# Performance work log

Hardware: AMD Instinct MI355X
Metric: run time of the kernel (lower is better)

Reference implementation:

```python
import jax, jax.numpy as jnp
import numpy as np
import math

N, E, H, NB, NL, NG, NELEM = 50000, 800000, 64, 8, 2, 64, 100
CUTOFF = 5.0


def _lin(k, fin, fout):
    kw, kb = jax.random.split(k)
    bound = 1.0 / math.sqrt(fin)
    w = jax.random.uniform(kw, (fin, fout), jnp.float32, -bound, bound)
    b = jax.random.uniform(kb, (fout,), jnp.float32, -bound, bound)
    return w, b


def setup_inputs() -> dict:
    key = jax.random.key(0)
    ks = jax.random.split(key, 12)
    z = jax.random.randint(ks[0], (N,), 0, NELEM)
    pos = jax.random.normal(ks[1], (N, 3), jnp.float32)
    edge_index = jax.random.randint(ks[2], (2, E), 0, N)
    batch = jnp.sort(jax.random.randint(ks[3], (N,), 0, NG))
    embed = jax.random.normal(ks[4], (NELEM, H), jnp.float32)
    # stacked per-interaction MLP params, leading dim = NL
    msg_w1, msg_b1, msg_w2, msg_b2 = [], [], [], []
    upd_w1, upd_b1, upd_w2, upd_b2 = [], [], [], []
    for l in range(NL):
        kl = jax.random.fold_in(ks[5], l)
        k1, k2, k3, k4 = jax.random.split(kl, 4)
        w, b = _lin(k1, 2 * H + NB, H); msg_w1.append(w); msg_b1.append(b)
        w, b = _lin(k2, H, H); msg_w2.append(w); msg_b2.append(b)
        w, b = _lin(k3, 2 * H, H); upd_w1.append(w); upd_b1.append(b)
        w, b = _lin(k4, H, H); upd_w2.append(w); upd_b2.append(b)
    eh_w1, eh_b1 = _lin(ks[6], H, H)
    eh_w2, eh_b2 = _lin(ks[7], H, 1)
    return {
        "z": z, "pos": pos, "edge_index": edge_index, "batch": batch,
        "embed": embed,
        "msg_w1": jnp.stack(msg_w1), "msg_b1": jnp.stack(msg_b1),
        "msg_w2": jnp.stack(msg_w2), "msg_b2": jnp.stack(msg_b2),
        "upd_w1": jnp.stack(upd_w1), "upd_b1": jnp.stack(upd_b1),
        "upd_w2": jnp.stack(upd_w2), "upd_b2": jnp.stack(upd_b2),
        "eh_w1": eh_w1, "eh_b1": eh_b1, "eh_w2": eh_w2, "eh_b2": eh_b2,
    }


def _mace_energy(pos, embed, msg_w1, msg_b1, msg_w2, msg_b2,
                 upd_w1, upd_b1, upd_w2, upd_b2,
                 eh_w1, eh_b1, eh_w2, eh_b2,
                 z, edge_index, batch):
    row, col = edge_index[0], edge_index[1]
    edge_vec = pos[row] - pos[col]                      # (E,3)
    d = jnp.linalg.norm(edge_vec, axis=-1)              # (E,)
    env = jnp.where(d < CUTOFF,
                    jnp.cos(d * (math.pi / (2 * CUTOFF))) ** 2,
                    0.0)
    freqs = jnp.arange(1, NB + 1, dtype=pos.dtype) * (math.pi / CUTOFF)
    d_safe = jnp.where(d > 0, d, 1.0)[:, None]
    edge_attr = jnp.sin(freqs * d[:, None]) / d_safe * env[:, None]  # (E,NB)

    x = embed[z]                                        # (N,H)
    for l in range(NL):
        # PyG source_to_target: x_j = x[row], x_i = x[col], aggregate at col
        msg_in = jnp.concatenate([x[col], x[row], edge_attr], axis=-1)  # (E,2H+NB)
        m = jax.nn.silu(msg_in @ msg_w1[l] + msg_b1[l]) @ msg_w2[l] + msg_b2[l]
        agg = jax.ops.segment_sum(m, col, num_segments=N)               # (N,H)
        u_in = jnp.concatenate([x, agg], axis=-1)
        upd = jax.nn.silu(u_in @ upd_w1[l] + upd_b1[l]) @ upd_w2[l] + upd_b2[l]
        x = x + upd

    atomic_e = jax.nn.silu(x @ eh_w1 + eh_b1) @ eh_w2 + eh_b2           # (N,1)
    energy = jax.ops.segment_sum(atomic_e, batch, num_segments=NG)      # (NG,1)
    return energy.squeeze(-1)


def reference(z, pos, edge_index, batch, embed,
              msg_w1, msg_b1, msg_w2, msg_b2,
              upd_w1, upd_b1, upd_w2, upd_b2,
              eh_w1, eh_b1, eh_w2, eh_b2):
    return _mace_energy(pos, embed, msg_w1, msg_b1, msg_w2, msg_b2,
                        upd_w1, upd_b1, upd_w2, upd_b2,
                        eh_w1, eh_b1, eh_w2, eh_b2,
                        z, edge_index, batch)
```

## Files before the change

kernel.cpp:

```cpp
#include <hip/hip_runtime.h>
#include <math.h>

#define NN 50000
#define EE 800000
#define HH 64
#define NBASIS 8
#define NLAYER 2
#define NGRAPH 64
#define NBLK1 49

using half2_t = decltype(__builtin_amdgcn_cvt_pkrtz(0.0f, 0.0f));
typedef _Float16 f16x8 __attribute__((ext_vector_type(8)));
typedef float f32x4 __attribute__((ext_vector_type(4)));

union U4H8 { uint4 u; f16x8 h; };

__device__ __forceinline__ float silu_f(float v) {
    return v * (1.0f / (1.0f + __expf(-v)));
}

__device__ __forceinline__ unsigned pk2(float a, float b) {
    union { half2_t h; unsigned u; } x;
    x.h = __builtin_amdgcn_cvt_pkrtz(a, b);
    return x.u;
}

__device__ __forceinline__ half2_t u2h(unsigned u) {
    union { unsigned u; half2_t h; } x; x.u = u; return x.h;
}

__global__ __launch_bounds__(256) void prep_k(
    const int* __restrict__ z, const float* __restrict__ embed,
    unsigned* __restrict__ xh,
    const float* __restrict__ msg_w1, const float* __restrict__ msg_w2,
    const float* __restrict__ msg_b2,
    const float* __restrict__ upd_w1, const float* __restrict__ upd_w2,
    const float* __restrict__ eh_w1,
    unsigned* __restrict__ w1t, float* __restrict__ vbuf,
    unsigned* __restrict__ w1tu, unsigned* __restrict__ w2tu,
    unsigned* __restrict__ ehw1t,
    const int* __restrict__ ecol, int* __restrict__ deg,
    float4* __restrict__ agg4)
{
    int b = blockIdx.x;
    if (b < 6250) {
        int idx = b * 256 + threadIdx.x;
        int n = idx >> 5;
        int p = idx & 31;
        const float2* er = (const float2*)(embed + ((size_t)z[n] << 6));
        float2 v = er[p];
        xh[idx] = pk2(v.x, v.y);
    } else if (b < 6362) {
        int idx = (b - 6250) * 256 + threadIdx.x;
        if (idx < 10240) {
            int l = idx / 5120, rem = idx % 5120;
            int f = rem / 80, kp = rem % 80;
            const float* w = msg_w1 + (size_t)l * 136 * 64;
            unsigned v = 0;
            if (kp < 68) v = pk2(w[(2*kp)*64 + f], w[(2*kp+1)*64 + f]);
            w1t[idx] = v;
        } else if (idx < 14336) {
        } else if (idx < 22528) {
            int j = idx - 14336;
            int l = j / 4096, rem = j % 4096;
            int f = rem >> 6, kp = rem & 63;
            const float* w = upd_w1 + (size_t)l * 128 * 64;
            unsigned outv;
            if (kp < 32) {
                outv = pk2(w[(2*kp)*64 + f], w[(2*kp+1)*64 + f]);
            } else {
                const float* w2m = msg_w2 + (size_t)l * 64 * 64;
                int j0 = 2 * kp - 64;
                float v0 = 0.0f, v1 = 0.0f;
                for (int k = 0; k < 64; ++k) {
                    float wa = w[(64 + k) * 64 + f];
                    v0 += w2m[j0 * 64 + k]       * wa;
                    v1 += w2m[(j0 + 1) * 64 + k] * wa;
                }
                outv = pk2(v0, v1);
                if (kp == 63) {
                    const float* b2m = msg_b2 + (size_t)l * 64;
                    float s = 0.0f;
                    for (int k = 0; k < 64; ++k)
                        s += b2m[k] * w[(64 + k) * 64 + f];
                    vbuf[l * 64 + f] = s;
                }
            }
            w1tu[j] = outv;
        } else if (idx < 26624) {
            int j = idx - 22528;
            int l = j / 2048, rem = j % 2048;
            int n = rem / 32, kp = rem % 32;
            const float* w = upd_w2 + (size_t)l * 64 * 64;
            w2tu[j] = pk2(w[(2*kp)*64 + n], w[(2*kp+1)*64 + n]);
        } else if (idx < 28672) {
            int j = idx - 26624;
            int f = j / 32, kp = j % 32;
            ehw1t[j] = pk2(eh_w1[(2*kp)*64 + f], eh_w1[(2*kp+1)*64 + f]);
        }
    } else if (b < 9487) {
        int e = (b - 6362) * 256 + threadIdx.x;
        if (e < EE) atomicAdd(&deg[ecol[e]], 1);
    } else {
        int idx = (b - 9487) * 256 + threadIdx.x;
        if (idx < NN * 16) {
            float4 z4; z4.x = z4.y = z4.z = z4.w = 0.0f;
            agg4[idx] = z4;
        }
    }
}

__global__ __launch_bounds__(1024) void scan1_k(
    const int* __restrict__ deg, int* __restrict__ cursor,
    int* __restrict__ bsum)
{
    __shared__ int wsum[16];
    int t = threadIdx.x, lane = t & 63, wave = t >> 6;
    int i = blockIdx.x * 1024 + t;
    int v = (i < NN) ? deg[i] : 0;
    int s = v;
#pragma unroll
    for (int off = 1; off < 64; off <<= 1) {
        int tv = __shfl_up(s, off, 64);
        if (lane >= off) s += tv;
    }
    if (lane == 63) wsum[wave] = s;
    __syncthreads();
    if (wave == 0) {
        int ws = (lane < 16) ? wsum[lane] : 0;
        int ss = ws;
#pragma unroll
        for (int off = 1; off < 16; off <<= 1) {
            int tv = __shfl_up(ss, off, 64);
            if (lane >= off) ss += tv;
        }
        if (lane < 16) wsum[lane] = ss - ws;
    }
    __syncthreads();
    int excl = wsum[wave] + s - v;
    if (i < NN) cursor[i] = excl;
    if (t == 1023) bsum[blockIdx.x] = excl + v;
}

__global__ __launch_bounds__(64) void scan2_k(int* __restrict__ bsum)
{
    int lane = threadIdx.x;
    int v = (lane < NBLK1) ? bsum[lane] : 0;
    int s = v;
#pragma unroll
    for (int off = 1; off < 64; off <<= 1) {
        int tv = __shfl_up(s, off, 64);
        if (lane >= off) s += tv;
    }
    if (lane < NBLK1) bsum[lane] = s - v;
}

__global__ __launch_bounds__(256) void scatter_k(
    const int* __restrict__ erow, const int* __restrict__ ecol,
    const float* __restrict__ pos,
    int* __restrict__ cursor, const int* __restrict__ bsum,
    uint2* __restrict__ edgeS)
{
    int e = blockIdx.x * 256 + threadIdx.x;
    if (e >= EE) return;
    int c = ecol[e], r = erow[e];
    int slot = atomicAdd(&cursor[c], 1) + bsum[c >> 10];
    float dx = pos[3*r]   - pos[3*c];
    float dy = pos[3*r+1] - pos[3*c+1];
    float dz = pos[3*r+2] - pos[3*c+2];
    float d = sqrtf(dx*dx + dy*dy + dz*dz);
    uint2 v;
    v.x = ((unsigned)r << 16) | (unsigned)c;
    v.y = __float_as_uint(d);
    edgeS[slot] = v;
}

__global__ __launch_bounds__(256, 4) void msg_k(
    const uint2* __restrict__ edgeS,
    const unsigned* __restrict__ xh,
    const unsigned* __restrict__ w1t, const float* __restrict__ b1,
    float* __restrict__ agg)
{
    __shared__ unsigned earrT[4][4 * 64];
    __shared__ int ckey_s[4][64];
    __shared__ float Mbuf[4][64 * 34];

    const int wid  = threadIdx.x >> 6;
    const int lane = threadIdx.x & 63;
    const int q = lane >> 4, n15 = lane & 15;
    const size_t base = (size_t)blockIdx.x * 256 + wid * 64;

    uint2 ev = edgeS[base + lane];
    int myrow = (int)(ev.x >> 16);
    int mykey = (int)(ev.x & 0xffffu);
    ckey_s[wid][lane] = mykey;

    int cn[4], rn[4];
#pragma unroll
    for (int nt = 0; nt < 4; ++nt) {
        cn[nt] = __shfl(mykey, nt * 16 + n15, 64);
        rn[nt] = __shfl(myrow, nt * 16 + n15, 64);
    }

    U4H8 bfr[2][4];
#pragma unroll
    for (int nt = 0; nt < 4; ++nt) {
        const uint4* rp = (const uint4*)(xh + ((size_t)rn[nt] << 5));
        bfr[0][nt].u = rp[q];
        bfr[1][nt].u = rp[4 + q];
    }

    {
        float d = __uint_as_float(ev.y);
        float env = 0.0f;
        if (d < 5.0f) {
            float cv = __cosf(d * 0.31415926535897932f);
            env = cv * cv;
        }
        float scale = (d > 0.0f) ? (env / d) : env;
        float ea[NBASIS];
#pragma unroll
        for (int k = 0; k < NBASIS; ++k)
            ea[k] = __sinf((float)(k + 1) * 0.62831853071795865f * d) * scale;
#pragma unroll
        for (int p = 0; p < 4; ++p)
            earrT[wid][p * 64 + lane] = pk2(ea[2*p], ea[2*p+1]);
    }
    int pkk = __shfl_up(mykey, 1, 64);
    unsigned long long bmask = __ballot(lane > 0 && mykey != pkk);
    unsigned m32 = (unsigned)(bmask >> (lane & 32));
    __syncthreads();

    f32x4 acc1[4][4];
#pragma unroll
    for (int mt = 0; mt < 4; ++mt) {
        f32x4 binit = *(const f32x4*)(b1 + mt * 16 + q * 4);
#pragma unroll
        for (int nt = 0; nt < 4; ++nt) acc1[mt][nt] = binit;
    }
#pragma unroll
    for (int ks = 0; ks < 5; ++ks) {
        U4H8 bfk[4];
#pragma unroll
        for (int nt = 0; nt < 4; ++nt) {
            if (ks == 4) {
                int eB = nt * 16 + n15;
                unsigned e0 = earrT[wid][0 * 64 + eB];
                unsigned e1 = earrT[wid][1 * 64 + eB];
                unsigned e2 = earrT[wid][2 * 64 + eB];
                unsigned e3 = earrT[wid][3 * 64 + eB];
                bfk[nt].u.x = (q == 0) ? e0 : 0u;
                bfk[nt].u.y = (q == 0) ? e1 : 0u;
                bfk[nt].u.z = (q == 0) ? e2 : 0u;
                bfk[nt].u.w = (q == 0) ? e3 : 0u;
            } else if (ks < 2) {
                bfk[nt].u = ((const uint4*)(xh + ((size_t)cn[nt] << 5)))[ks * 4 + q];
            } else {
                bfk[nt] = bfr[ks - 2][nt];
            }
        }
#pragma unroll
        for (int mt = 0; mt < 4; ++mt) {
            U4H8 af;
            af.u = *(const uint4*)(w1t + (size_t)(mt * 16 + n15) * 80 + ks * 16 + q * 4);
#pragma unroll
            for (int nt = 0; nt < 4; ++nt)
                acc1[mt][nt] = __builtin_amdgcn_mfma_f32_16x16x32_f16(
                    af.h, bfk[nt].h, acc1[mt][nt], 0, 0, 0);
        }
    }

#pragma unroll
    for (int hf = 0; hf < 2; ++hf) {
#pragma unroll
        for (int mh = 0; mh < 2; ++mh) {
            int mt = 2 * hf + mh;
#pragma unroll
            for (int nt = 0; nt < 4; ++nt) {
                int eb = nt * 16 + n15;
#pragma unroll
                for (int r = 0; r < 4; ++r)
                    Mbuf[wid][eb * 34 + mh * 16 + q * 4 + r] =
                        silu_f(acc1[mt][nt][r]);
            }
        }
        __syncthreads();
        {
            int cl = lane & 31, st = lane >> 5;
            int ebase = 32 * st;
            float run = Mbuf[wid][ebase * 34 + cl];
            int runkey = ckey_s[wid][ebase];
            bool atstart = true;
#pragma unroll
            for (int i = 1; i < 32; ++i) {
                float v = Mbuf[wid][(ebase + i) * 34 + cl];
                if ((m32 >> i) & 1u) {
                    float* dst = agg + ((size_t)runkey << 6) + hf * 32 + cl;
                    if (atstart) atomicAdd(dst, run); else *dst = run;
                    runkey = ckey_s[wid][ebase + i]; atstart = false;
                    run = v;
                } else {
                    run += v;
                }
            }
            atomicAdd(agg + ((size_t)runkey << 6) + hf * 32 + cl, run);
        }
        __syncthreads();
    }
}

__global__ __launch_bounds__(256) void upd_k(
    unsigned* __restrict__ xh,
    float* __restrict__ agg,
    const unsigned* __restrict__ w1t, const float* __restrict__ b1,
    const float* __restrict__ vb, const int* __restrict__ deg,
    const unsigned* __restrict__ w2t, const float* __restrict__ b2,
    const unsigned* __restrict__ ehw1t, const float* __restrict__ ehb1,
    const float* __restrict__ ehw2, const float* __restrict__ ehb2,
    const int* __restrict__ batch, float* __restrict__ energy,
    int do_zero, int do_head)
{
    __shared__ unsigned MU[4][16 * 33];
    __shared__ float esum[NGRAPH];

    const int tid = threadIdx.x;
    const int wid = tid >> 6;
    const int lane = tid & 63;
    const int q = lane >> 4, n15 = lane & 15;
    const int base16 = blockIdx.x * 64 + wid * 16;

    if (do_head) {
        if (tid < NGRAPH) esum[tid] = 0.0f;
        __syncthreads();
    }

    int nodeB = base16 + n15;
    int ncB = (nodeB < NN) ? nodeB : (NN - 1);

    float degf = (float)deg[ncB];
    f32x4 acc1[4];
#pragma unroll
    for (int mt = 0; mt < 4; ++mt) {
        f32x4 bi = *(const f32x4*)(b1 + mt * 16 + q * 4);
        f32x4 vv = *(const f32x4*)(vb + mt * 16 + q * 4);
#pragma unroll
        for (int r = 0; r < 4; ++r) bi[r] = fmaf(degf, vv[r], bi[r]);
        acc1[mt] = bi;
    }
#pragma unroll
    for (int ks = 0; ks < 4; ++ks) {
        U4H8 bfk;
        if (ks < 2) {
            bfk.u = ((const uint4*)(xh + ((size_t)ncB << 5)))[ks * 4 + q];
        } else {
            const float4* ap = (const float4*)(agg + ((size_t)ncB << 6));
            int o = (ks - 2) * 8 + 2 * q;
            float4 a0 = ap[o], a1 = ap[o + 1];
            bfk.u.x = pk2(a0.x, a0.y); bfk.u.y = pk2(a0.z, a0.w);
            bfk.u.z = pk2(a1.x, a1.y); bfk.u.w = pk2(a1.z, a1.w);
        }
#pragma unroll
        for (int mt = 0; mt < 4; ++mt) {
            U4H8 af;
            af.u = *(const uint4*)(w1t + (size_t)(mt * 16 + n15) * 64 + ks * 16 + q * 4);
            acc1[mt] = __builtin_amdgcn_mfma_f32_16x16x32_f16(
                af.h, bfk.h, acc1[mt], 0, 0, 0);
        }
    }

    unsigned psrc[4][2];
#pragma unroll
    for (int mt = 0; mt < 4; ++mt) {
        psrc[mt][0] = pk2(silu_f(acc1[mt][0]), silu_f(acc1[mt][1]));
        psrc[mt][1] = pk2(silu_f(acc1[mt][2]), silu_f(acc1[mt][3]));
    }

    f32x4 acc2[4];
#pragma unroll
    for (int nt = 0; nt < 4; ++nt) {
        float b2v = b2[nt * 16 + n15];
        acc2[nt][0] = b2v; acc2[nt][1] = b2v; acc2[nt][2] = b2v; acc2[nt][3] = b2v;
    }
#pragma unroll
    for (int ks2 = 0; ks2 < 2; ++ks2) {
        unsigned tmp[4];
#pragma unroll
        for (int jr = 0; jr < 4; ++jr) {
            int srcl = (2 * (q & 1) + (jr >> 1)) * 16 + n15;
            unsigned v0 = (unsigned)__shfl((int)psrc[2 * ks2][jr & 1], srcl, 64);
            unsigned v1 = (unsigned)__shfl((int)psrc[2 * ks2 + 1][jr & 1], srcl, 64);
            tmp[jr] = (q >> 1) ? v1 : v0;
        }
        U4H8 pf;
        pf.u.x = tmp[0]; pf.u.y = tmp[1]; pf.u.z = tmp[2]; pf.u.w = tmp[3];
#pragma unroll
        for (int nt = 0; nt < 4; ++nt) {
            U4H8 wb;
            wb.u = *(const uint4*)(w2t + (size_t)(nt * 16 + n15) * 32 + ks2 * 16 + q * 4);
            acc2[nt] = __builtin_amdgcn_mfma_f32_16x16x32_f16(
                pf.h, wb.h, acc2[nt], 0, 0, 0);
        }
    }

#pragma unroll
    for (int nt = 0; nt < 4; ++nt) {
#pragma unroll
        for (int r = 0; r < 4; ++r) {
            int node = base16 + 4 * q + r;
            float vnew = 0.0f;
            if (node < NN) {
                unsigned pu = xh[((size_t)node << 5) + (unsigned)((nt * 16 + n15) >> 1)];
                half2_t hp = u2h(pu);
                float vold = (n15 & 1) ? (float)hp[1] : (float)hp[0];
                vnew = vold + acc2[nt][r];
            }
            float vpart = __shfl_xor(vnew, 1, 64);
            if ((n15 & 1) == 0) {
                unsigned pv = pk2(vnew, vpart);
                int pidx = nt * 8 + (n15 >> 1);
                MU[wid][(4 * q + r) * 33 + pidx] = pv;
                if (node < NN) xh[((size_t)node << 5) + pidx] = pv;
            }
        }
    }

    if (do_zero) {
        if (nodeB < NN) {
            float4 z4; z4.x = z4.y = z4.z = z4.w = 0.0f;
            float4* ap = (float4*)(agg + ((size_t)nodeB << 6));
            ap[2*q] = z4; ap[2*q + 1] = z4;
            ap[8 + 2*q] = z4; ap[8 + 2*q + 1] = z4;
        }
    }

    if (do_head) {
        __syncthreads();
        f32x4 acch[4];
#pragma unroll
        for (int mt = 0; mt < 4; ++mt)
            acch[mt] = *(const f32x4*)(ehb1 + mt * 16 + q * 4);
#pragma unroll
        for (int ks = 0; ks < 2; ++ks) {
            U4H8 bfk;
            bfk.u.x = MU[wid][n15 * 33 + ks * 16 + 4 * q + 0];
            bfk.u.y = MU[wid][n15 * 33 + ks * 16 + 4 * q + 1];
            bfk.u.z = MU[wid][n15 * 33 + ks * 16 + 4 * q + 2];
            bfk.u.w = MU[wid][n15 * 33 + ks * 16 + 4 * q + 3];
#pragma unroll
            for (int mt = 0; mt < 4; ++mt) {
                U4H8 af;
                af.u = *(const uint4*)(ehw1t + (size_t)(mt * 16 + n15) * 32 + ks * 16 + q * 4);
                acch[mt] = __builtin_amdgcn_mfma_f32_16x16x32_f16(
                    af.h, bfk.h, acch[mt], 0, 0, 0);
            }
        }
        f32x4 wv[4];
#pragma unroll
        for (int mt = 0; mt < 4; ++mt)
            wv[mt] = *(const f32x4*)(ehw2 + mt * 16 + q * 4);
        float e = 0.0f;
#pragma unroll
        for (int mt = 0; mt < 4; ++mt)
#pragma unroll
            for (int r = 0; r < 4; ++r)
                e = fmaf(silu_f(acch[mt][r]), wv[mt][r], e);
        e += __shfl_xor(e, 16, 64);
        e += __shfl_xor(e, 32, 64);
        if (q == 0) {
            int node = base16 + n15;
            if (node < NN) atomicAdd(&esum[batch[node]], e + ehb2[0]);
        }
        __syncthreads();
        if (tid < NGRAPH) {
            float v = esum[tid];
            if (v != 0.0f) atomicAdd(energy + tid, v);
        }
    }
}

extern "C" void kernel_launch(void* const* d_in, const int* in_sizes, int n_in,
                              void* d_out, int out_size, void* d_ws, size_t ws_size,
                              hipStream_t stream) {
    const int*   z       = (const int*)  d_in[0];
    const float* pos     = (const float*)d_in[1];
    const int*   eidx    = (const int*)  d_in[2];
    const int*   batch   = (const int*)  d_in[3];
    const float* embed   = (const float*)d_in[4];
    const float* msg_w1  = (const float*)d_in[5];
    const float* msg_b1  = (const float*)d_in[6];
    const float* msg_w2  = (const float*)d_in[7];
    const float* msg_b2  = (const float*)d_in[8];
    const float* upd_w1  = (const float*)d_in[9];
    const float* upd_b1  = (const float*)d_in[10];
    const float* upd_w2  = (const float*)d_in[11];
    const float* upd_b2  = (const float*)d_in[12];
    const float* eh_w1   = (const float*)d_in[13];
    const float* eh_b1   = (const float*)d_in[14];
    const float* eh_w2   = (const float*)d_in[15];
    const float* eh_b2   = (const float*)d_in[16];

    const int* erow = eidx;
    const int* ecol = eidx + EE;

    float*    agg    = (float*)d_ws;
    unsigned* xh     = (unsigned*)(agg + (size_t)NN * HH);
    int*      deg    = (int*)(xh + (size_t)NN * 32);
    int*      cursor = deg + NN;
    int*      bsum   = cursor + NN;
    uint2*    edgeS  = (uint2*)(bsum + 64);
    unsigned* w1t    = (unsigned*)(edgeS + EE);
    unsigned* w2t    = w1t + NLAYER * 64 * 80;
    unsigned* w1tu   = w2t + NLAYER * 64 * 32;
    unsigned* w2tu   = w1tu + NLAYER * 64 * 64;
    unsigned* ehw1t  = w2tu + NLAYER * 64 * 32;
    float*    vbuf   = (float*)w2t;
    float*    energy = (float*)d_out;

    (void)hipMemsetAsync(energy, 0, NGRAPH * sizeof(float), stream);
    (void)hipMemsetAsync(deg, 0, NN * sizeof(int), stream);

    prep_k<<<12612, 256, 0, stream>>>(
        z, embed, xh,
        msg_w1, msg_w2, msg_b2, upd_w1, upd_w2, eh_w1,
        w1t, vbuf, w1tu, w2tu, ehw1t,
        ecol, deg, (float4*)agg);

    scan1_k<<<NBLK1, 1024, 0, stream>>>(deg, cursor, bsum);
    scan2_k<<<1, 64, 0, stream>>>(bsum);
    scatter_k<<<(EE + 255) / 256, 256, 0, stream>>>(
        erow, ecol, pos, cursor, bsum, edgeS);

    for (int l = 0; l < NLAYER; ++l) {
        msg_k<<<EE / 256, 256, 0, stream>>>(
            edgeS, xh,
            w1t + (size_t)l * 64 * 80,
            msg_b1 + (size_t)l * HH,
            agg);
        upd_k<<<(NN + 63) / 64, 256, 0, stream>>>(
            xh, agg,
            w1tu + (size_t)l * 64 * 64,
            upd_b1 + (size_t)l * HH,
            vbuf + (size_t)l * 64,
            deg,
            w2tu + (size_t)l * 64 * 32,
            upd_b2 + (size_t)l * HH,
            ehw1t, eh_b1, eh_w2, eh_b2, batch, energy,
            (l == 0) ? 1 : 0,
            (l == NLAYER - 1) ? 1 : 0);
    }
}
```

Baseline: 357.9 us.

## Pack silu messages as fp16 in swizzled LDS and segment-reduce in one pass

Replaces the edge-attribute and key shared arrays with register shuffles. The silu outputs are now stored as packed fp16 pairs in an XOR-swizzled shared buffer, so all 64 channels fit at once and the two-half reduction loop with its extra barriers collapses into a single pass. Each lane now reduces two channels. Run keys are re-read from global edgeS at segment boundaries. The cost is fp16 rounding of the messages before summation, which lowers precision, and extra global loads for the keys.

```diff
diff --git a/kernel.cpp b/kernel.cpp
--- a/kernel.cpp
+++ b/kernel.cpp
@@ -181,9 +181,7 @@
     const unsigned* __restrict__ w1t, const float* __restrict__ b1,
     float* __restrict__ agg)
 {
-    __shared__ unsigned earrT[4][4 * 64];
-    __shared__ int ckey_s[4][64];
-    __shared__ float Mbuf[4][64 * 34];
+    __shared__ unsigned Mbuf[4][64][32];
 
     const int wid  = threadIdx.x >> 6;
     const int lane = threadIdx.x & 63;
@@ -193,7 +191,6 @@
     uint2 ev = edgeS[base + lane];
     int myrow = (int)(ev.x >> 16);
     int mykey = (int)(ev.x & 0xffffu);
-    ckey_s[wid][lane] = mykey;
 
     int cn[4], rn[4];
 #pragma unroll
@@ -210,6 +207,7 @@
         bfr[1][nt].u = rp[4 + q];
     }
 
+    unsigned ep0, ep1, ep2, ep3;
     {
         float d = __uint_as_float(ev.y);
         float env = 0.0f;
@@ -222,9 +220,8 @@
 #pragma unroll
         for (int k = 0; k < NBASIS; ++k)
             ea[k] = __sinf((float)(k + 1) * 0.62831853071795865f * d) * scale;
-#pragma unroll
-        for (int p = 0; p < 4; ++p)
-            earrT[wid][p * 64 + lane] = pk2(ea[2*p], ea[2*p+1]);
+        ep0 = pk2(ea[0], ea[1]); ep1 = pk2(ea[2], ea[3]);
+        ep2 = pk2(ea[4], ea[5]); ep3 = pk2(ea[6], ea[7]);
     }
     int pkk = __shfl_up(mykey, 1, 64);
     unsigned long long bmask = __ballot(lane > 0 && mykey != pkk);
@@ -245,10 +242,10 @@
         for (int nt = 0; nt < 4; ++nt) {
             if (ks == 4) {
                 int eB = nt * 16 + n15;
-                unsigned e0 = earrT[wid][0 * 64 + eB];
-                unsigned e1 = earrT[wid][1 * 64 + eB];
-                unsigned e2 = earrT[wid][2 * 64 + eB];
-                unsigned e3 = earrT[wid][3 * 64 + eB];
+                unsigned e0 = (unsigned)__shfl((int)ep0, eB, 64);
+                unsigned e1 = (unsigned)__shfl((int)ep1, eB, 64);
+                unsigned e2 = (unsigned)__shfl((int)ep2, eB, 64);
+                unsigned e3 = (unsigned)__shfl((int)ep3, eB, 64);
                 bfk[nt].u.x = (q == 0) ? e0 : 0u;
                 bfk[nt].u.y = (q == 0) ? e1 : 0u;
                 bfk[nt].u.z = (q == 0) ? e2 : 0u;
@@ -271,41 +268,41 @@
     }
 
 #pragma unroll
-    for (int hf = 0; hf < 2; ++hf) {
-#pragma unroll
-        for (int mh = 0; mh < 2; ++mh) {
-            int mt = 2 * hf + mh;
-#pragma unroll
-            for (int nt = 0; nt < 4; ++nt) {
-                int eb = nt * 16 + n15;
-#pragma unroll
-                for (int r = 0; r < 4; ++r)
-                    Mbuf[wid][eb * 34 + mh * 16 + q * 4 + r] =
-                        silu_f(acc1[mt][nt][r]);
+    for (int mt = 0; mt < 4; ++mt)
+#pragma unroll
+        for (int nt = 0; nt < 4; ++nt) {
+            unsigned w0 = pk2(silu_f(acc1[mt][nt][0]), silu_f(acc1[mt][nt][1]));
+            unsigned w1 = pk2(silu_f(acc1[mt][nt][2]), silu_f(acc1[mt][nt][3]));
+            int e = 16 * nt + n15;
+            int sl = (mt * 8 + 2 * q) ^ (n15 << 1);
+            uint2 wv; wv.x = w0; wv.y = w1;
+            *(uint2*)&Mbuf[wid][e][sl] = wv;
+        }
+    __syncthreads();
+
+    {
+        int cl = lane & 31, st = lane >> 5;
+        int ebase = 32 * st;
+        int runkey = __shfl(mykey, ebase, 64);
+        half2_t h0 = u2h(Mbuf[wid][ebase][cl ^ 0]);
+        float run0 = (float)h0[0], run1 = (float)h0[1];
+        bool atstart = true;
+#pragma unroll
+        for (int i = 1; i < 32; ++i) {
+            half2_t hh = u2h(Mbuf[wid][ebase + i][cl ^ ((i & 15) << 1)]);
+            if ((m32 >> i) & 1u) {
+                float* dst = agg + ((size_t)runkey << 6) + 2 * cl;
+                if (atstart) { atomicAdd(dst, run0); atomicAdd(dst + 1, run1); }
+                else         { dst[0] = run0; dst[1] = run1; }
+                runkey = (int)(edgeS[base + ebase + i].x & 0xffffu);
+                atstart = false;
+                run0 = (float)hh[0]; run1 = (float)hh[1];
+            } else {
+                run0 += (float)hh[0]; run1 += (float)hh[1];
             }
         }
-        __syncthreads();
-        {
-            int cl = lane & 31, st = lane >> 5;
-            int ebase = 32 * st;
-            float run = Mbuf[wid][ebase * 34 + cl];
-            int runkey = ckey_s[wid][ebase];
-            bool atstart = true;
-#pragma unroll
-            for (int i = 1; i < 32; ++i) {
-                float v = Mbuf[wid][(ebase + i) * 34 + cl];
-                if ((m32 >> i) & 1u) {
-                    float* dst = agg + ((size_t)runkey << 6) + hf * 32 + cl;
-                    if (atstart) atomicAdd(dst, run); else *dst = run;
-                    runkey = ckey_s[wid][ebase + i]; atstart = false;
-                    run = v;
-                } else {
-                    run += v;
-                }
-            }
-            atomicAdd(agg + ((size_t)runkey << 6) + hf * 32 + cl, run);
-        }
-        __syncthreads();
+        float* dst = agg + ((size_t)runkey << 6) + 2 * cl;
+        atomicAdd(dst, run0); atomicAdd(dst + 1, run1);
     }
 }
 
```

Result: slower. 382.7 us (+6.9%).

## Swap MFMA operand roles and do segmented reduction in registers instead of LDS

Applied to the files above, without the earlier changes.

The message kernel now puts edges on the MFMA M dimension and features on N, so each lane holds accumulators for 16 consecutive edges of one feature column. The segmented sum over sorted destination keys then runs in registers, with a cross-quad shuffle scan handling carries. This removes the Mbuf shared-memory staging buffer, its two __syncthreads per half and the LDS traffic. The cost is more complex boundary logic mixing atomics and plain stores, which carries correctness risk, plus extra shuffles.

```diff
diff --git a/kernel.cpp b/kernel.cpp
--- a/kernel.cpp
+++ b/kernel.cpp
@@ -183,7 +183,6 @@
 {
     __shared__ unsigned earrT[4][4 * 64];
     __shared__ int ckey_s[4][64];
-    __shared__ float Mbuf[4][64 * 34];
 
     const int wid  = threadIdx.x >> 6;
     const int lane = threadIdx.x & 63;
@@ -195,19 +194,21 @@
     int mykey = (int)(ev.x & 0xffffu);
     ckey_s[wid][lane] = mykey;
 
+    const int oo0 = 16 * (n15 >> 2) + (n15 & 3);
+
     int cn[4], rn[4];
 #pragma unroll
-    for (int nt = 0; nt < 4; ++nt) {
-        cn[nt] = __shfl(mykey, nt * 16 + n15, 64);
-        rn[nt] = __shfl(myrow, nt * 16 + n15, 64);
+    for (int et = 0; et < 4; ++et) {
+        cn[et] = __shfl(mykey, oo0 + 4 * et, 64);
+        rn[et] = __shfl(myrow, oo0 + 4 * et, 64);
     }
 
     U4H8 bfr[2][4];
 #pragma unroll
-    for (int nt = 0; nt < 4; ++nt) {
-        const uint4* rp = (const uint4*)(xh + ((size_t)rn[nt] << 5));
-        bfr[0][nt].u = rp[q];
-        bfr[1][nt].u = rp[4 + q];
+    for (int et = 0; et < 4; ++et) {
+        const uint4* rp = (const uint4*)(xh + ((size_t)rn[et] << 5));
+        bfr[0][et].u = rp[q];
+        bfr[1][et].u = rp[4 + q];
     }
 
     {
@@ -228,84 +229,142 @@
     }
     int pkk = __shfl_up(mykey, 1, 64);
     unsigned long long bmask = __ballot(lane > 0 && mykey != pkk);
-    unsigned m32 = (unsigned)(bmask >> (lane & 32));
     __syncthreads();
 
     f32x4 acc1[4][4];
 #pragma unroll
-    for (int mt = 0; mt < 4; ++mt) {
-        f32x4 binit = *(const f32x4*)(b1 + mt * 16 + q * 4);
-#pragma unroll
-        for (int nt = 0; nt < 4; ++nt) acc1[mt][nt] = binit;
+    for (int ft = 0; ft < 4; ++ft) {
+        float bv = b1[ft * 16 + n15];
+        f32x4 binit; binit[0] = bv; binit[1] = bv; binit[2] = bv; binit[3] = bv;
+#pragma unroll
+        for (int et = 0; et < 4; ++et) acc1[et][ft] = binit;
     }
 #pragma unroll
     for (int ks = 0; ks < 5; ++ks) {
-        U4H8 bfk[4];
-#pragma unroll
-        for (int nt = 0; nt < 4; ++nt) {
+        U4H8 afrag[4];
+#pragma unroll
+        for (int et = 0; et < 4; ++et) {
             if (ks == 4) {
-                int eB = nt * 16 + n15;
+                int eB = oo0 + 4 * et;
                 unsigned e0 = earrT[wid][0 * 64 + eB];
                 unsigned e1 = earrT[wid][1 * 64 + eB];
                 unsigned e2 = earrT[wid][2 * 64 + eB];
                 unsigned e3 = earrT[wid][3 * 64 + eB];
-                bfk[nt].u.x = (q == 0) ? e0 : 0u;
-                bfk[nt].u.y = (q == 0) ? e1 : 0u;
-                bfk[nt].u.z = (q == 0) ? e2 : 0u;
-                bfk[nt].u.w = (q == 0) ? e3 : 0u;
+                afrag[et].u.x = (q == 0) ? e0 : 0u;
+                afrag[et].u.y = (q == 0) ? e1 : 0u;
+                afrag[et].u.z = (q == 0) ? e2 : 0u;
+                afrag[et].u.w = (q == 0) ? e3 : 0u;
             } else if (ks < 2) {
-                bfk[nt].u = ((const uint4*)(xh + ((size_t)cn[nt] << 5)))[ks * 4 + q];
+                afrag[et].u = ((const uint4*)(xh + ((size_t)cn[et] << 5)))[ks * 4 + q];
             } else {
-                bfk[nt] = bfr[ks - 2][nt];
-            }
-        }
-#pragma unroll
-        for (int mt = 0; mt < 4; ++mt) {
-            U4H8 af;
-            af.u = *(const uint4*)(w1t + (size_t)(mt * 16 + n15) * 80 + ks * 16 + q * 4);
-#pragma unroll
-            for (int nt = 0; nt < 4; ++nt)
-                acc1[mt][nt] = __builtin_amdgcn_mfma_f32_16x16x32_f16(
-                    af.h, bfk[nt].h, acc1[mt][nt], 0, 0, 0);
-        }
-    }
-
-#pragma unroll
-    for (int hf = 0; hf < 2; ++hf) {
-#pragma unroll
-        for (int mh = 0; mh < 2; ++mh) {
-            int mt = 2 * hf + mh;
-#pragma unroll
-            for (int nt = 0; nt < 4; ++nt) {
-                int eb = nt * 16 + n15;
-#pragma unroll
-                for (int r = 0; r < 4; ++r)
-                    Mbuf[wid][eb * 34 + mh * 16 + q * 4 + r] =
-                        silu_f(acc1[mt][nt][r]);
-            }
-        }
-        __syncthreads();
-        {
-            int cl = lane & 31, st = lane >> 5;
-            int ebase = 32 * st;
-            float run = Mbuf[wid][ebase * 34 + cl];
-            int runkey = ckey_s[wid][ebase];
-            bool atstart = true;
-#pragma unroll
-            for (int i = 1; i < 32; ++i) {
-                float v = Mbuf[wid][(ebase + i) * 34 + cl];
-                if ((m32 >> i) & 1u) {
-                    float* dst = agg + ((size_t)runkey << 6) + hf * 32 + cl;
-                    if (atstart) atomicAdd(dst, run); else *dst = run;
-                    runkey = ckey_s[wid][ebase + i]; atstart = false;
-                    run = v;
-                } else {
-                    run += v;
-                }
-            }
-            atomicAdd(agg + ((size_t)runkey << 6) + hf * 32 + cl, run);
-        }
-        __syncthreads();
+                afrag[et] = bfr[ks - 2][et];
+            }
+        }
+#pragma unroll
+        for (int ft = 0; ft < 4; ++ft) {
+            U4H8 wf;
+            wf.u = *(const uint4*)(w1t + (size_t)(ft * 16 + n15) * 80 + ks * 16 + q * 4);
+#pragma unroll
+            for (int et = 0; et < 4; ++et)
+                acc1[et][ft] = __builtin_amdgcn_mfma_f32_16x16x32_f16(
+                    afrag[et].h, wf.h, acc1[et][ft], 0, 0, 0);
+        }
+    }
+
+    unsigned myb = (unsigned)((bmask >> (16 * q)) & 0xffffull);
+    const bool bstart = (myb & 1u) != 0;
+    float run[4], hs[4];
+#pragma unroll
+    for (int ft = 0; ft < 4; ++ft) run[ft] = silu_f(acc1[0][ft][0]);
+    bool seenb = false; int fb = 0;
+#pragma unroll
+    for (int i = 1; i < 16; ++i) {
+        float vv[4];
+#pragma unroll
+        for (int ft = 0; ft < 4; ++ft) vv[ft] = silu_f(acc1[i >> 2][ft][i & 3]);
+        if ((myb >> i) & 1u) {
+            if (!seenb) {
+                seenb = true; fb = i;
+#pragma unroll
+                for (int ft = 0; ft < 4; ++ft) hs[ft] = run[ft];
+            } else {
+                int kk = ckey_s[wid][16 * q + i - 1];
+                float* dst = agg + ((size_t)kk << 6) + n15;
+#pragma unroll
+                for (int ft = 0; ft < 4; ++ft) dst[16 * ft] = run[ft];
+            }
+#pragma unroll
+            for (int ft = 0; ft < 4; ++ft) run[ft] = vv[ft];
+        } else {
+#pragma unroll
+            for (int ft = 0; ft < 4; ++ft) run[ft] += vv[ft];
+        }
+    }
+
+    float ct[4];
+#pragma unroll
+    for (int ft = 0; ft < 4; ++ft) ct[ft] = run[ft];
+    int brk = (seenb || bstart) ? 1 : 0;
+    {
+        float cp[4]; int bp;
+#pragma unroll
+        for (int ft = 0; ft < 4; ++ft) cp[ft] = __shfl_up(ct[ft], 16, 64);
+        bp = __shfl_up(brk, 16, 64);
+        if (q >= 1) {
+            if (!brk) {
+#pragma unroll
+                for (int ft = 0; ft < 4; ++ft) ct[ft] += cp[ft];
+            }
+            brk |= bp;
+        }
+#pragma unroll
+        for (int ft = 0; ft < 4; ++ft) cp[ft] = __shfl_up(ct[ft], 32, 64);
+        bp = __shfl_up(brk, 32, 64);
+        if (q >= 2) {
+            if (!brk) {
+#pragma unroll
+                for (int ft = 0; ft < 4; ++ft) ct[ft] += cp[ft];
+            }
+            brk |= bp;
+        }
+    }
+    float carry[4];
+#pragma unroll
+    for (int ft = 0; ft < 4; ++ft) carry[ft] = __shfl_up(ct[ft], 16, 64);
+    const bool headflag = (q == 0) ||
+        ((bmask & (((unsigned long long)1 << (16 * q)) - 2)) == 0ull);
+
+    if (q > 0 && bstart) {
+        int kk = ckey_s[wid][16 * q - 1];
+        float* dst = agg + ((size_t)kk << 6) + n15;
+        if (headflag) {
+#pragma unroll
+            for (int ft = 0; ft < 4; ++ft) atomicAdd(dst + 16 * ft, carry[ft]);
+        } else {
+#pragma unroll
+            for (int ft = 0; ft < 4; ++ft) dst[16 * ft] = carry[ft];
+        }
+    }
+    if (seenb) {
+        int kk = ckey_s[wid][16 * q + fb - 1];
+        float* dst = agg + ((size_t)kk << 6) + n15;
+        if (!bstart && q > 0) {
+#pragma unroll
+            for (int ft = 0; ft < 4; ++ft) hs[ft] += carry[ft];
+        }
+        if (headflag && !bstart) {
+#pragma unroll
+            for (int ft = 0; ft < 4; ++ft) atomicAdd(dst + 16 * ft, hs[ft]);
+        } else {
+#pragma unroll
+            for (int ft = 0; ft < 4; ++ft) dst[16 * ft] = hs[ft];
+        }
+    }
+    if (q == 3) {
+        int kk = ckey_s[wid][63];
+        float* dst = agg + ((size_t)kk << 6) + n15;
+#pragma unroll
+        for (int ft = 0; ft < 4; ++ft) atomicAdd(dst + 16 * ft, ct[ft]);
     }
 }
 
```

After: 345.8 us. -3.4%, faster.
